# Kernel optimization log

Measured on AMD Instinct MI355X. Metric: run time of the kernel, lower is better.

The kernel has to match this reference:

```python
import jax, jax.numpy as jnp
import numpy as np

B, T, C, H = 2, 2048, 1024, 16
HD = C // H  # 64

def setup_inputs() -> dict:
    key = jax.random.key(0)
    ks = jax.random.split(key, 9)
    s = 0.02
    return {
        "x": jax.random.normal(ks[0], (B, T, C), jnp.float32),
        "Wq": jax.random.normal(ks[1], (C, C), jnp.float32) * s,
        "bq": jax.random.normal(ks[2], (C,), jnp.float32) * s,
        "Wk": jax.random.normal(ks[3], (C, C), jnp.float32) * s,
        "bk": jax.random.normal(ks[4], (C,), jnp.float32) * s,
        "Wv": jax.random.normal(ks[5], (C, C), jnp.float32) * s,
        "bv": jax.random.normal(ks[6], (C,), jnp.float32) * s,
        "Wp": jax.random.normal(ks[7], (C, C), jnp.float32) * s,
        "bp": jax.random.normal(ks[8], (C,), jnp.float32) * s,
    }

def reference(x, Wq, bq, Wk, bk, Wv, bv, Wp, bp):
    Bb, Tt, Cc = x.shape
    hd = Cc // H
    # project and split heads: [B, H, T, hd]
    def heads(W, b):
        return (x @ W.T + b).reshape(Bb, Tt, H, hd).transpose(0, 2, 1, 3)
    q, k, v = heads(Wq, bq), heads(Wk, bk), heads(Wv, bv)
    scale = 1.0 / np.sqrt(hd).astype(np.float32)
    att = jnp.einsum('bhqd,bhkd->bhqk', q, k) * scale
    causal = jnp.tril(jnp.ones((Tt, Tt), bool))
    att = jnp.where(causal[None, None], att, -jnp.inf)
    att = jax.nn.softmax(att, axis=-1)
    y = jnp.einsum('bhqk,bhkd->bhqd', att, v)
    y = y.transpose(0, 2, 1, 3).reshape(Bb, Tt, Cc)
    return y @ Wp.T + bp
```

## Files before the change

kernel.cpp:

```cpp
#include <hip/hip_runtime.h>
#include <hip/hip_bf16.h>

#define Tsz 2048
#define Csz 1024
#define Hn 16

typedef short s8v __attribute__((ext_vector_type(8)));
typedef short s4v __attribute__((ext_vector_type(4)));
typedef float f4v __attribute__((ext_vector_type(4)));

#define QSCALE (0.125f * 1.44269504088896f)

__device__ __forceinline__ short bf_bits(float x) {
    __hip_bfloat16 t = __float2bfloat16(x);
    return *reinterpret_cast<short*>(&t);
}

__device__ __forceinline__ void gload_lds(const void* g, void* l) {
    __builtin_amdgcn_global_load_lds(
        (const __attribute__((address_space(1))) void*)g,
        (__attribute__((address_space(3))) void*)l, 16, 0, 0);
}

__global__ void cvt5(const float* __restrict__ x, const float* __restrict__ wq,
                     const float* __restrict__ wk, const float* __restrict__ wv,
                     const float* __restrict__ wp,
                     short* __restrict__ xo, short* __restrict__ qo,
                     short* __restrict__ ko, short* __restrict__ vo,
                     short* __restrict__ po) {
    const int y = blockIdx.y;
    const float* in; short* out; int n;
    switch (y) {
        case 0: in = x;  out = xo; n = 2 * Tsz * Csz; break;
        case 1: in = wq; out = qo; n = Csz * Csz; break;
        case 2: in = wk; out = ko; n = Csz * Csz; break;
        case 3: in = wv; out = vo; n = Csz * Csz; break;
        default: in = wp; out = po; n = Csz * Csz; break;
    }
    int i = (blockIdx.x * blockDim.x + threadIdx.x) * 4;
    if (i >= n) return;
    float4 v = *(const float4*)(in + i);
    short4 o;
    o.x = bf_bits(v.x); o.y = bf_bits(v.y); o.z = bf_bits(v.z); o.w = bf_bits(v.w);
    *(short4*)(out + i) = o;
}

__global__ __launch_bounds__(256, 3) void qkv_gemm(
    const short* __restrict__ X,
    const short* __restrict__ Wq, const short* __restrict__ Wk, const short* __restrict__ Wv,
    const float* __restrict__ bq, const float* __restrict__ bk, const float* __restrict__ bv,
    short* __restrict__ Qo, short* __restrict__ Ko, short* __restrict__ Vto)
{
    const int z = blockIdx.z;
    const short* W = (z == 0) ? Wq : (z == 1) ? Wk : Wv;
    const float* bias = (z == 0) ? bq : (z == 1) ? bk : bv;

    __shared__ __align__(16) short Ash[128 * 32];
    __shared__ __align__(16) short Bsh[128 * 32];
    __shared__ __align__(16) short TR[64 * 72];

    const int tid = threadIdx.x, lane = tid & 63, wave = tid >> 6;
    const int ln = lane & 15, hi = lane >> 4;
    const int m0 = blockIdx.x * 128, n0 = blockIdx.y * 128;
    const int wm = (wave >> 1) * 64, wn = (wave & 1) * 64;

    const short* Ag = X + (size_t)(m0 + (tid >> 2)) * Csz + (tid & 3) * 8;
    const short* Bg = W + (size_t)(n0 + (tid >> 2)) * Csz + (tid & 3) * 8;

    f4v acc[4][4];
    #pragma unroll
    for (int mt = 0; mt < 4; mt++)
        #pragma unroll
        for (int nt = 0; nt < 4; nt++)
            #pragma unroll
            for (int i = 0; i < 4; i++) acc[mt][nt][i] = 0.f;

    for (int k0 = 0; k0 < Csz; k0 += 32) {
        __syncthreads();
        gload_lds(Ag + k0, Ash + tid * 8);
        gload_lds(Ag + k0 + (size_t)64 * Csz, Ash + 2048 + tid * 8);
        gload_lds(Bg + k0, Bsh + tid * 8);
        gload_lds(Bg + k0 + (size_t)64 * Csz, Bsh + 2048 + tid * 8);
        __syncthreads();

        s8v af[4], bfr[4];
        #pragma unroll
        for (int mt = 0; mt < 4; mt++)
            af[mt] = *(const s8v*)(Ash + (wm + mt * 16 + ln) * 32 + hi * 8);
        #pragma unroll
        for (int nt = 0; nt < 4; nt++)
            bfr[nt] = *(const s8v*)(Bsh + (wn + nt * 16 + ln) * 32 + hi * 8);
        #pragma unroll
        for (int mt = 0; mt < 4; mt++)
            #pragma unroll
            for (int nt = 0; nt < 4; nt++)
                acc[mt][nt] = __builtin_amdgcn_mfma_f32_16x16x32_bf16(af[mt], bfr[nt], acc[mt][nt], 0, 0, 0);
    }

    if (z == 2) {
        const int b = m0 >> 11, t0 = m0 & 2047;
        float bvv[4];
        #pragma unroll
        for (int nt = 0; nt < 4; nt++) bvv[nt] = bias[n0 + wn + nt * 16 + ln];
        #pragma unroll
        for (int ph = 0; ph < 4; ph++) {
            const int mh = ph >> 1, nh = ph & 1;
            __syncthreads();
            if ((wave >> 1) == mh && (wave & 1) == nh) {
                #pragma unroll
                for (int mt = 0; mt < 4; mt++)
                    #pragma unroll
                    for (int nt = 0; nt < 4; nt++) {
                        s4v pk;
                        #pragma unroll
                        for (int i = 0; i < 4; i++) pk[i] = bf_bits(acc[mt][nt][i] + bvv[nt]);
                        *(s4v*)(TR + (nt * 16 + ln) * 72 + mt * 16 + hi * 4) = pk;
                    }
            }
            __syncthreads();
            const int chl = tid >> 2, seg = tid & 3;
            const s8v r0 = *(const s8v*)(TR + chl * 72 + seg * 16);
            const s8v r1 = *(const s8v*)(TR + chl * 72 + seg * 16 + 8);
            short* dst = Vto + (size_t)(b * 1024 + n0 + nh * 64 + chl) * Tsz + t0 + mh * 64 + seg * 16;
            *(s8v*)(dst) = r0;
            *(s8v*)(dst + 8) = r1;
        }
        return;
    }

    const float scale = (z == 0) ? QSCALE : 1.0f;
    short* out = (z == 0) ? Qo : Ko;

    #pragma unroll
    for (int nt = 0; nt < 4; nt++) {
        const int col = n0 + wn + nt * 16 + ln;
        const float bvv = bias[col];
        #pragma unroll
        for (int mt = 0; mt < 4; mt++) {
            const int row0 = m0 + wm + mt * 16 + hi * 4;
            #pragma unroll
            for (int i = 0; i < 4; i++)
                out[(size_t)(row0 + i) * Csz + col] = bf_bits((acc[mt][nt][i] + bvv) * scale);
        }
    }
}

__global__ __launch_bounds__(256, 2) void proj_gemm(
    const short* __restrict__ A, const short* __restrict__ W,
    const float* __restrict__ bias, float* __restrict__ out)
{
    __shared__ __align__(16) short Ash[128 * 32];
    __shared__ __align__(16) short Bsh[64 * 32];

    const int tid = threadIdx.x, lane = tid & 63, wave = tid >> 6;
    const int ln = lane & 15, hi = lane >> 4;
    const int m0 = blockIdx.x * 128, n0 = blockIdx.y * 64;
    const int wm = (wave >> 1) * 64, wn = (wave & 1) * 32;

    const short* Ag = A + (size_t)(m0 + (tid >> 2)) * Csz + (tid & 3) * 8;
    const short* Bg = W + (size_t)(n0 + (tid >> 2)) * Csz + (tid & 3) * 8;

    f4v acc[4][2];
    #pragma unroll
    for (int mt = 0; mt < 4; mt++)
        #pragma unroll
        for (int nt = 0; nt < 2; nt++)
            #pragma unroll
            for (int i = 0; i < 4; i++) acc[mt][nt][i] = 0.f;

    for (int k0 = 0; k0 < Csz; k0 += 32) {
        __syncthreads();
        gload_lds(Ag + k0, Ash + tid * 8);
        gload_lds(Ag + k0 + (size_t)64 * Csz, Ash + 2048 + tid * 8);
        gload_lds(Bg + k0, Bsh + tid * 8);
        __syncthreads();

        s8v af[4], bfr[2];
        #pragma unroll
        for (int mt = 0; mt < 4; mt++)
            af[mt] = *(const s8v*)(Ash + (wm + mt * 16 + ln) * 32 + hi * 8);
        #pragma unroll
        for (int nt = 0; nt < 2; nt++)
            bfr[nt] = *(const s8v*)(Bsh + (wn + nt * 16 + ln) * 32 + hi * 8);
        #pragma unroll
        for (int mt = 0; mt < 4; mt++)
            #pragma unroll
            for (int nt = 0; nt < 2; nt++)
                acc[mt][nt] = __builtin_amdgcn_mfma_f32_16x16x32_bf16(af[mt], bfr[nt], acc[mt][nt], 0, 0, 0);
    }

    #pragma unroll
    for (int nt = 0; nt < 2; nt++) {
        const int col = n0 + wn + nt * 16 + ln;
        const float bvv = bias[col];
        #pragma unroll
        for (int mt = 0; mt < 4; mt++)
            #pragma unroll
            for (int i = 0; i < 4; i++)
                out[(size_t)(m0 + wm + mt * 16 + hi * 4 + i) * Csz + col] = acc[mt][nt][i] + bvv;
    }
}

__global__ __launch_bounds__(256, 2) void attn6(
    const short* __restrict__ Q, const short* __restrict__ Kg,
    const short* __restrict__ Vt, short* __restrict__ Y)
{
    __shared__ __align__(16) short Ksh[64 * 72];
    __shared__ __align__(16) short Vsh[64 * 72];
    __shared__ __align__(16) short Psh[4][16 * 72];

    const int tid = threadIdx.x, lane = tid & 63, wave = tid >> 6;
    const int ln = lane & 15, hi = lane >> 4;
    const int p = blockIdx.x;
    const int qts[2] = { p, 31 - p };
    const int bh = blockIdx.y;
    const size_t base = (size_t)(bh >> 4) * Tsz * Csz + (size_t)(bh & 15) * 64;
    const size_t vtbase = (size_t)bh * 64 * Tsz;
    const int qrel = wave * 16 + ln;
    short* Pq = Psh[wave];

    s8v qf[2][2];
    #pragma unroll
    for (int t = 0; t < 2; t++)
        #pragma unroll
        for (int kk = 0; kk < 2; kk++)
            qf[t][kk] = *(const s8v*)(Q + base + (size_t)(qts[t] * 64 + qrel) * Csz + kk * 32 + hi * 8);

    f4v o[2][4];
    float lsum[2] = {0.f, 0.f};
    #pragma unroll
    for (int t = 0; t < 2; t++)
        #pragma unroll
        for (int dt = 0; dt < 4; dt++)
            #pragma unroll
            for (int i = 0; i < 4; i++) o[t][dt][i] = 0.f;

    const int sr = tid >> 2, sc = (tid & 3) * 16;
    const short* Kp = Kg + base + (size_t)sr * Csz + sc;
    const short* Vp = Vt + vtbase + (size_t)sr * Tsz + sc;
    short* KshW = Ksh + sr * 72 + sc;
    short* VshW = Vsh + sr * 72 + sc;

    const int nkb = qts[1] + 1;
    s8v ka  = *(const s8v*)(Kp);
    s8v kb2 = *(const s8v*)(Kp + 8);
    s8v va  = *(const s8v*)(Vp);
    s8v vb2 = *(const s8v*)(Vp + 8);

    for (int kb = 0; kb < nkb; kb++) {
        __syncthreads();
        *(s8v*)(KshW) = ka; *(s8v*)(KshW + 8) = kb2;
        *(s8v*)(VshW) = va; *(s8v*)(VshW + 8) = vb2;
        __syncthreads();

        const int knx = (kb + 1 < nkb) ? (kb + 1) * 64 : kb * 64;
        ka  = *(const s8v*)(Kp + (size_t)knx * Csz);
        kb2 = *(const s8v*)(Kp + (size_t)knx * Csz + 8);
        va  = *(const s8v*)(Vp + knx);
        vb2 = *(const s8v*)(Vp + knx + 8);

        s8v kf[2][4], vf[2][4];
        #pragma unroll
        for (int nt = 0; nt < 4; nt++)
            #pragma unroll
            for (int kk = 0; kk < 2; kk++) {
                kf[kk][nt] = *(const s8v*)(Ksh + (nt * 16 + ln) * 72 + kk * 32 + hi * 8);
                vf[kk][nt] = *(const s8v*)(Vsh + (nt * 16 + ln) * 72 + kk * 32 + hi * 8);
            }

        #pragma unroll
        for (int t = 0; t < 2; t++) {
            if (t == 0 && kb > qts[0]) continue;
            const bool dg = (kb == qts[t]);

            f4v s[4];
            #pragma unroll
            for (int nt = 0; nt < 4; nt++) {
                #pragma unroll
                for (int i = 0; i < 4; i++) s[nt][i] = 0.f;
                s[nt] = __builtin_amdgcn_mfma_f32_16x16x32_bf16(kf[0][nt], qf[t][0], s[nt], 0, 0, 0);
                s[nt] = __builtin_amdgcn_mfma_f32_16x16x32_bf16(kf[1][nt], qf[t][1], s[nt], 0, 0, 0);
            }

            #pragma unroll
            for (int nt = 0; nt < 4; nt++) {
                float pv[4];
                #pragma unroll
                for (int i = 0; i < 4; i++) pv[i] = exp2f(s[nt][i]);
                if (dg) {
                    const int kr = nt * 16 + hi * 4;
                    #pragma unroll
                    for (int i = 0; i < 4; i++)
                        if (kr + i > qrel) pv[i] = 0.f;
                }
                lsum[t] += (pv[0] + pv[1]) + (pv[2] + pv[3]);
                s4v w;
                #pragma unroll
                for (int i = 0; i < 4; i++) w[i] = bf_bits(pv[i]);
                *(s4v*)(Pq + ln * 72 + nt * 16 + hi * 4) = w;
            }
            const s8v pb0 = *(const s8v*)(Pq + ln * 72 + hi * 8);
            const s8v pb1 = *(const s8v*)(Pq + ln * 72 + 32 + hi * 8);

            #pragma unroll
            for (int dt = 0; dt < 4; dt++) {
                o[t][dt] = __builtin_amdgcn_mfma_f32_16x16x32_bf16(vf[0][dt], pb0, o[t][dt], 0, 0, 0);
                o[t][dt] = __builtin_amdgcn_mfma_f32_16x16x32_bf16(vf[1][dt], pb1, o[t][dt], 0, 0, 0);
            }
        }
    }

    #pragma unroll
    for (int t = 0; t < 2; t++) {
        float l = lsum[t];
        l += __shfl_xor(l, 16);
        l += __shfl_xor(l, 32);
        const float inv = 1.0f / l;
        const int qrow = qts[t] * 64 + qrel;
        #pragma unroll
        for (int dt = 0; dt < 4; dt++) {
            s4v w;
            #pragma unroll
            for (int i = 0; i < 4; i++) w[i] = bf_bits(o[t][dt][i] * inv);
            *(s4v*)(Y + base + (size_t)qrow * Csz + dt * 16 + hi * 4) = w;
        }
    }
}

extern "C" void kernel_launch(void* const* d_in, const int* in_sizes, int n_in,
                              void* d_out, int out_size, void* d_ws, size_t ws_size,
                              hipStream_t stream) {
    const float* x  = (const float*)d_in[0];
    const float* Wq = (const float*)d_in[1];
    const float* bq = (const float*)d_in[2];
    const float* Wk = (const float*)d_in[3];
    const float* bk = (const float*)d_in[4];
    const float* Wv = (const float*)d_in[5];
    const float* bv = (const float*)d_in[6];
    const float* Wp = (const float*)d_in[7];
    const float* bp = (const float*)d_in[8];

    char* ws = (char*)d_ws;
    short* Xb  = (short*)(ws);
    short* Wqb = (short*)(ws + (8u  << 20));
    short* Wkb = (short*)(ws + (10u << 20));
    short* Wvb = (short*)(ws + (12u << 20));
    short* Wpb = (short*)(ws + (14u << 20));
    short* Qb  = (short*)(ws + (16u << 20));
    short* Kb  = (short*)(ws + (24u << 20));
    short* Vtb = (short*)(ws + (32u << 20));
    short* Yb  = (short*)(ws + (40u << 20));

    hipLaunchKernelGGL(cvt5, dim3(4096, 5), dim3(256), 0, stream,
                       x, Wq, Wk, Wv, Wp, Xb, Wqb, Wkb, Wvb, Wpb);

    hipLaunchKernelGGL(qkv_gemm, dim3(32, 8, 3), dim3(256), 0, stream,
                       Xb, Wqb, Wkb, Wvb, bq, bk, bv, Qb, Kb, Vtb);

    hipLaunchKernelGGL(attn6, dim3(16, 32), dim3(256), 0, stream, Qb, Kb, Vtb, Yb);

    hipLaunchKernelGGL(proj_gemm, dim3(32, 16), dim3(256), 0, stream, Yb, Wpb, bp, (float*)d_out);
}
```

Measured before the change: 192.3 us.

## Double-buffer attention K/V with 512-thread blocks, widen proj tile, compact cvt grid

The attention kernel now runs two 4-wave groups per 512-thread block. Each group handles a balanced pair of causal query tiles, and the groups share one double-buffered K/V tile in LDS, which removes one barrier per iteration and overlaps the global loads. The projection GEMM moves to 128x128 tiles to get more MFMA work per LDS load, at the cost of higher register pressure and half as many blocks. The conversion kernel uses an exactly sized 1D grid so it no longer launches idle blocks for the weight matrices.

```diff
diff --git a/kernel.cpp b/kernel.cpp
--- a/kernel.cpp
+++ b/kernel.cpp
@@ -22,23 +22,26 @@
         (__attribute__((address_space(3))) void*)l, 16, 0, 0);
 }
 
-__global__ void cvt5(const float* __restrict__ x, const float* __restrict__ wq,
+__global__ void cvt6(const float* __restrict__ x, const float* __restrict__ wq,
                      const float* __restrict__ wk, const float* __restrict__ wv,
                      const float* __restrict__ wp,
                      short* __restrict__ xo, short* __restrict__ qo,
                      short* __restrict__ ko, short* __restrict__ vo,
                      short* __restrict__ po) {
-    const int y = blockIdx.y;
-    const float* in; short* out; int n;
-    switch (y) {
-        case 0: in = x;  out = xo; n = 2 * Tsz * Csz; break;
-        case 1: in = wq; out = qo; n = Csz * Csz; break;
-        case 2: in = wk; out = ko; n = Csz * Csz; break;
-        case 3: in = wv; out = vo; n = Csz * Csz; break;
-        default: in = wp; out = po; n = Csz * Csz; break;
-    }
-    int i = (blockIdx.x * blockDim.x + threadIdx.x) * 4;
-    if (i >= n) return;
+    const int bx = blockIdx.x;
+    const float* in; short* out; int ib;
+    if (bx < 4096) { in = x; out = xo; ib = bx; }
+    else {
+        const int r = bx - 4096, w = r >> 10;
+        ib = r & 1023;
+        switch (w) {
+            case 0: in = wq; out = qo; break;
+            case 1: in = wk; out = ko; break;
+            case 2: in = wv; out = vo; break;
+            default: in = wp; out = po; break;
+        }
+    }
+    const int i = ib * 1024 + threadIdx.x * 4;
     float4 v = *(const float4*)(in + i);
     short4 o;
     o.x = bf_bits(v.x); o.y = bf_bits(v.y); o.z = bf_bits(v.z); o.w = bf_bits(v.w);
@@ -150,21 +153,21 @@
     const float* __restrict__ bias, float* __restrict__ out)
 {
     __shared__ __align__(16) short Ash[128 * 32];
-    __shared__ __align__(16) short Bsh[64 * 32];
+    __shared__ __align__(16) short Bsh[128 * 32];
 
     const int tid = threadIdx.x, lane = tid & 63, wave = tid >> 6;
     const int ln = lane & 15, hi = lane >> 4;
-    const int m0 = blockIdx.x * 128, n0 = blockIdx.y * 64;
-    const int wm = (wave >> 1) * 64, wn = (wave & 1) * 32;
+    const int m0 = blockIdx.x * 128, n0 = blockIdx.y * 128;
+    const int wm = (wave >> 1) * 64, wn = (wave & 1) * 64;
 
     const short* Ag = A + (size_t)(m0 + (tid >> 2)) * Csz + (tid & 3) * 8;
     const short* Bg = W + (size_t)(n0 + (tid >> 2)) * Csz + (tid & 3) * 8;
 
-    f4v acc[4][2];
+    f4v acc[4][4];
     #pragma unroll
     for (int mt = 0; mt < 4; mt++)
         #pragma unroll
-        for (int nt = 0; nt < 2; nt++)
+        for (int nt = 0; nt < 4; nt++)
             #pragma unroll
             for (int i = 0; i < 4; i++) acc[mt][nt][i] = 0.f;
 
@@ -173,24 +176,25 @@
         gload_lds(Ag + k0, Ash + tid * 8);
         gload_lds(Ag + k0 + (size_t)64 * Csz, Ash + 2048 + tid * 8);
         gload_lds(Bg + k0, Bsh + tid * 8);
-        __syncthreads();
-
-        s8v af[4], bfr[2];
+        gload_lds(Bg + k0 + (size_t)64 * Csz, Bsh + 2048 + tid * 8);
+        __syncthreads();
+
+        s8v af[4], bfr[4];
         #pragma unroll
         for (int mt = 0; mt < 4; mt++)
             af[mt] = *(const s8v*)(Ash + (wm + mt * 16 + ln) * 32 + hi * 8);
         #pragma unroll
-        for (int nt = 0; nt < 2; nt++)
+        for (int nt = 0; nt < 4; nt++)
             bfr[nt] = *(const s8v*)(Bsh + (wn + nt * 16 + ln) * 32 + hi * 8);
         #pragma unroll
         for (int mt = 0; mt < 4; mt++)
             #pragma unroll
-            for (int nt = 0; nt < 2; nt++)
+            for (int nt = 0; nt < 4; nt++)
                 acc[mt][nt] = __builtin_amdgcn_mfma_f32_16x16x32_bf16(af[mt], bfr[nt], acc[mt][nt], 0, 0, 0);
     }
 
     #pragma unroll
-    for (int nt = 0; nt < 2; nt++) {
+    for (int nt = 0; nt < 4; nt++) {
         const int col = n0 + wn + nt * 16 + ln;
         const float bvv = bias[col];
         #pragma unroll
@@ -201,22 +205,23 @@
     }
 }
 
-__global__ __launch_bounds__(256, 2) void attn6(
+__global__ __launch_bounds__(512, 2) void attn7(
     const short* __restrict__ Q, const short* __restrict__ Kg,
     const short* __restrict__ Vt, short* __restrict__ Y)
 {
-    __shared__ __align__(16) short Ksh[64 * 72];
-    __shared__ __align__(16) short Vsh[64 * 72];
-    __shared__ __align__(16) short Psh[4][16 * 72];
+    __shared__ __align__(16) short Ksh[2][64 * 72];
+    __shared__ __align__(16) short Vsh[2][64 * 72];
+    __shared__ __align__(16) short Psh[8][16 * 72];
 
     const int tid = threadIdx.x, lane = tid & 63, wave = tid >> 6;
+    const int wv = wave & 3, g = wave >> 2;
     const int ln = lane & 15, hi = lane >> 4;
     const int p = blockIdx.x;
-    const int qts[2] = { p, 31 - p };
+    const int qts[2] = { g ? 15 - p : p, g ? 16 + p : 31 - p };
     const int bh = blockIdx.y;
     const size_t base = (size_t)(bh >> 4) * Tsz * Csz + (size_t)(bh & 15) * 64;
     const size_t vtbase = (size_t)bh * 64 * Tsz;
-    const int qrel = wave * 16 + ln;
+    const int qrel = wv * 16 + ln;
     short* Pq = Psh[wave];
 
     s8v qf[2][2];
@@ -235,42 +240,43 @@
             #pragma unroll
             for (int i = 0; i < 4; i++) o[t][dt][i] = 0.f;
 
-    const int sr = tid >> 2, sc = (tid & 3) * 16;
+    const int sr = tid >> 3, sc = (tid & 7) * 8;
     const short* Kp = Kg + base + (size_t)sr * Csz + sc;
     const short* Vp = Vt + vtbase + (size_t)sr * Tsz + sc;
-    short* KshW = Ksh + sr * 72 + sc;
-    short* VshW = Vsh + sr * 72 + sc;
-
-    const int nkb = qts[1] + 1;
-    s8v ka  = *(const s8v*)(Kp);
-    s8v kb2 = *(const s8v*)(Kp + 8);
-    s8v va  = *(const s8v*)(Vp);
-    s8v vb2 = *(const s8v*)(Vp + 8);
+    const int swo = sr * 72 + sc;
+
+    const int nkb = 32 - p;
+
+    s8v kR = *(const s8v*)(Kp);
+    s8v vR = *(const s8v*)(Vp);
+    *(s8v*)(&Ksh[0][swo]) = kR;
+    *(s8v*)(&Vsh[0][swo]) = vR;
+    kR = *(const s8v*)(Kp + (size_t)64 * Csz);
+    vR = *(const s8v*)(Vp + 64);
+    __syncthreads();
 
     for (int kb = 0; kb < nkb; kb++) {
-        __syncthreads();
-        *(s8v*)(KshW) = ka; *(s8v*)(KshW + 8) = kb2;
-        *(s8v*)(VshW) = va; *(s8v*)(VshW + 8) = vb2;
-        __syncthreads();
-
-        const int knx = (kb + 1 < nkb) ? (kb + 1) * 64 : kb * 64;
-        ka  = *(const s8v*)(Kp + (size_t)knx * Csz);
-        kb2 = *(const s8v*)(Kp + (size_t)knx * Csz + 8);
-        va  = *(const s8v*)(Vp + knx);
-        vb2 = *(const s8v*)(Vp + knx + 8);
+        const int buf = kb & 1;
+        if (kb + 1 < nkb) {
+            *(s8v*)(&Ksh[buf ^ 1][swo]) = kR;
+            *(s8v*)(&Vsh[buf ^ 1][swo]) = vR;
+            const int knx = (kb + 2 < nkb) ? (kb + 2) * 64 : (nkb - 1) * 64;
+            kR = *(const s8v*)(Kp + (size_t)knx * Csz);
+            vR = *(const s8v*)(Vp + knx);
+        }
 
         s8v kf[2][4], vf[2][4];
         #pragma unroll
         for (int nt = 0; nt < 4; nt++)
             #pragma unroll
             for (int kk = 0; kk < 2; kk++) {
-                kf[kk][nt] = *(const s8v*)(Ksh + (nt * 16 + ln) * 72 + kk * 32 + hi * 8);
-                vf[kk][nt] = *(const s8v*)(Vsh + (nt * 16 + ln) * 72 + kk * 32 + hi * 8);
+                kf[kk][nt] = *(const s8v*)(&Ksh[buf][(nt * 16 + ln) * 72 + kk * 32 + hi * 8]);
+                vf[kk][nt] = *(const s8v*)(&Vsh[buf][(nt * 16 + ln) * 72 + kk * 32 + hi * 8]);
             }
 
         #pragma unroll
         for (int t = 0; t < 2; t++) {
-            if (t == 0 && kb > qts[0]) continue;
+            if (kb > qts[t]) continue;
             const bool dg = (kb == qts[t]);
 
             f4v s[4];
@@ -308,6 +314,7 @@
                 o[t][dt] = __builtin_amdgcn_mfma_f32_16x16x32_bf16(vf[1][dt], pb1, o[t][dt], 0, 0, 0);
             }
         }
+        __syncthreads();
     }
 
     #pragma unroll
@@ -351,13 +358,13 @@
     short* Vtb = (short*)(ws + (32u << 20));
     short* Yb  = (short*)(ws + (40u << 20));
 
-    hipLaunchKernelGGL(cvt5, dim3(4096, 5), dim3(256), 0, stream,
+    hipLaunchKernelGGL(cvt6, dim3(8192), dim3(256), 0, stream,
                        x, Wq, Wk, Wv, Wp, Xb, Wqb, Wkb, Wvb, Wpb);
 
     hipLaunchKernelGGL(qkv_gemm, dim3(32, 8, 3), dim3(256), 0, stream,
                        Xb, Wqb, Wkb, Wvb, bq, bk, bv, Qb, Kb, Vtb);
 
-    hipLaunchKernelGGL(attn6, dim3(16, 32), dim3(256), 0, stream, Qb, Kb, Vtb, Yb);
-
-    hipLaunchKernelGGL(proj_gemm, dim3(32, 16), dim3(256), 0, stream, Yb, Wpb, bp, (float*)d_out);
-}
+    hipLaunchKernelGGL(attn7, dim3(8, 32), dim3(512), 0, stream, Qb, Kb, Vtb, Yb);
+
+    hipLaunchKernelGGL(proj_gemm, dim3(32, 8), dim3(256), 0, stream, Yb, Wpb, bp, (float*)d_out);
+}
```

After: 191.4 us. About the same (-0.5%).
